# Optimization experiments

Measured on AMD Instinct MI355X. Metric: run time of the kernel, lower is better.

Reference implementation:

```python
import jax, jax.numpy as jnp
import numpy as np

L, B, N, D, H, INTER = 4, 64, 128, 1024, 16, 4096
HD = D // H
EPS = 1e-12


def layer_norm(x, g, b):
    m = jnp.mean(x, axis=-1, keepdims=True)
    v = jnp.mean(jnp.square(x - m), axis=-1, keepdims=True)
    return (x - m) * jax.lax.rsqrt(v + EPS) * g + b


def fast_self_attention(x, wq_w, wq_b, wk_w, wk_b, hwq, hwk, tr_w, tr_b):
    # x: [B, T, D]
    Bq, T, _ = x.shape
    q = x @ wq_w + wq_b                                  # [B,T,D]
    hq = q.reshape(Bq, T, H, HD).transpose(0, 2, 1, 3)    # [B,H,T,hd]
    # additive attention over queries (mask scores are all-zero here)
    alpha = jax.nn.softmax(jnp.einsum('bhtd,hd->bht', hq, hwq) / np.sqrt(HD), axis=-1)
    gq = jnp.einsum('bht,bhtd->bhd', alpha, hq).reshape(Bq, 1, D)  # global query [B,1,D]
    k = x @ wk_w + wk_b
    p = k * gq                                            # [B,T,D]
    hp = p.reshape(Bq, T, H, HD).transpose(0, 2, 1, 3)
    beta = jax.nn.softmax(jnp.einsum('bhtd,hd->bht', hp, hwk) / np.sqrt(HD), axis=-1)
    gk = jnp.einsum('bht,bhtd->bhd', beta, hp).reshape(Bq, 1, D)   # global key [B,1,D]
    u = q * gk
    r = u @ tr_w + tr_b
    return r + q


def encoder_layer(x, p, i):
    a = fast_self_attention(x, p['wq_w'][i], p['wq_b'][i], p['wk_w'][i], p['wk_b'][i],
                            p['hwq'][i], p['hwk'][i], p['tr_w'][i], p['tr_b'][i])
    a = a @ p['so_w'][i] + p['so_b'][i]
    a = layer_norm(a, p['ln1_g'][i], p['ln1_b'][i])
    h = jax.nn.gelu(a @ p['int_w'][i] + p['int_b'][i], approximate=False)
    o = h @ p['out_w'][i] + p['out_b'][i]
    return layer_norm(o + a, p['ln2_g'][i], p['ln2_b'][i])


def setup_inputs() -> dict:
    key = jax.random.key(0)
    ks = iter(jax.random.split(key, 32))
    s = 0.02
    inp = {
        'x': jax.random.normal(next(ks), (B, N, D), jnp.float32),
        'wq_w': jax.random.normal(next(ks), (L, D, D)) * s,
        'wq_b': jnp.zeros((L, D)),
        'wk_w': jax.random.normal(next(ks), (L, D, D)) * s,
        'wk_b': jnp.zeros((L, D)),
        'hwq': jax.random.normal(next(ks), (L, H, HD)) * s,
        'hwk': jax.random.normal(next(ks), (L, H, HD)) * s,
        'tr_w': jax.random.normal(next(ks), (L, D, D)) * s,
        'tr_b': jnp.zeros((L, D)),
        'so_w': jax.random.normal(next(ks), (L, D, D)) * s,
        'so_b': jnp.zeros((L, D)),
        'ln1_g': jnp.ones((L, D)),
        'ln1_b': jnp.zeros((L, D)),
        'int_w': jax.random.normal(next(ks), (L, D, INTER)) * s,
        'int_b': jnp.zeros((L, INTER)),
        'out_w': jax.random.normal(next(ks), (L, INTER, D)) * s,
        'out_b': jnp.zeros((L, D)),
        'ln2_g': jnp.ones((L, D)),
        'ln2_b': jnp.zeros((L, D)),
        'pool_w': jax.random.normal(next(ks), (D, D)) * s,
        'pool_b': jnp.zeros((D,)),
        'pool_q': jax.random.normal(next(ks), (D,)) * s,
    }
    return inp


def reference(x, wq_w, wq_b, wk_w, wk_b, hwq, hwk, tr_w, tr_b, so_w, so_b,
              ln1_g, ln1_b, int_w, int_b, out_w, out_b, ln2_g, ln2_b,
              pool_w, pool_b, pool_q):
    p = dict(wq_w=wq_w, wq_b=wq_b, wk_w=wk_w, wk_b=wk_b, hwq=hwq, hwk=hwk,
             tr_w=tr_w, tr_b=tr_b, so_w=so_w, so_b=so_b, ln1_g=ln1_g, ln1_b=ln1_b,
             int_w=int_w, int_b=int_b, out_w=out_w, out_b=out_b, ln2_g=ln2_g, ln2_b=ln2_b)
    h = x
    for i in range(L):
        h = encoder_layer(h, p, i)
    # additive attention pooling (mask scores are zeros)
    scores = jnp.tanh(h @ pool_w + pool_b) @ pool_q       # [B,N]
    w = jax.nn.softmax(scores, axis=-1)
    return jnp.einsum('bn,bnd->bd', w, h)                 # [B,D]
```

## Files before the change

### kernel.cpp

```cpp
#include <hip/hip_runtime.h>
#include <hip/hip_bf16.h>
#include <math.h>

typedef unsigned short u16;
typedef __attribute__((ext_vector_type(4))) unsigned short u16x4;
typedef __attribute__((ext_vector_type(8))) unsigned short u16x8;
typedef __attribute__((ext_vector_type(8))) short s16x8;
typedef __attribute__((ext_vector_type(4))) float f32x4;

typedef const __attribute__((address_space(1))) void* gas_t;
typedef __attribute__((address_space(3))) void* las_t;

#define DI __device__ __forceinline__

static constexpr int Bc = 64, Nc = 128, Dc = 1024, Hc = 16, HDc = 64, Ic = 4096, Lc = 4;
static constexpr int Mrows = Bc * Nc;

DI float b2f(u16 u) { union { unsigned i; float f; } x; x.i = ((unsigned)u) << 16; return x.f; }
DI u16 f2b(float f) {
  union { float f; unsigned i; } x; x.f = f;
  unsigned r = x.i + 0x7FFF + ((x.i >> 16) & 1);
  return (u16)(r >> 16);
}

#define BARRIER do { asm volatile("" ::: "memory"); __builtin_amdgcn_s_barrier(); asm volatile("" ::: "memory"); } while (0)
#define VMC(N) asm volatile("s_waitcnt vmcnt(" #N ")" ::: "memory")

#define STG(PTR, ROW0, T, SLOT) do { \
    const u16* _s = (PTR) + (size_t)((ROW0) + srow) * K + (((T) << 6) + scol); \
    __builtin_amdgcn_global_load_lds((gas_t)_s, (las_t)(smem + (SLOT) + ldsw), 16, 0, 0); \
    __builtin_amdgcn_global_load_lds((gas_t)(_s + ((size_t)K << 3)), (las_t)(smem + (SLOT) + ldsw + 1024), 16, 0, 0); \
  } while (0)

#define LDA(BUFB, RH) do { \
    _Pragma("unroll") \
    for (int mi = 0; mi < 4; ++mi) { \
      af[mi][0] = *(const s16x8*)(smem + (BUFB) + Abase_rd + (RH) * 8192 + mi * 2048 + aoff0); \
      af[mi][1] = *(const s16x8*)(smem + (BUFB) + Abase_rd + (RH) * 8192 + mi * 2048 + aoff1); \
    } } while (0)

#define LDB(DST, BUFB, CH) do { \
    _Pragma("unroll") \
    for (int nj = 0; nj < 2; ++nj) { \
      DST[nj][0] = *(const s16x8*)(smem + (BUFB) + Bbase_rd + (CH) * 4096 + nj * 2048 + aoff0); \
      DST[nj][1] = *(const s16x8*)(smem + (BUFB) + Bbase_rd + (CH) * 4096 + nj * 2048 + aoff1); \
    } } while (0)

#define MFMAQ(RH, CH, BF) do { \
    __builtin_amdgcn_s_setprio(1); \
    _Pragma("unroll") \
    for (int mi = 0; mi < 4; ++mi) \
      _Pragma("unroll") \
      for (int nj = 0; nj < 2; ++nj) { \
        acc[(RH) * 4 + mi][(CH) * 2 + nj] = __builtin_amdgcn_mfma_f32_16x16x32_bf16( \
            af[mi][0], BF[nj][0], acc[(RH) * 4 + mi][(CH) * 2 + nj], 0, 0, 0); \
        acc[(RH) * 4 + mi][(CH) * 2 + nj] = __builtin_amdgcn_mfma_f32_16x16x32_bf16( \
            af[mi][1], BF[nj][1], acc[(RH) * 4 + mi][(CH) * 2 + nj], 0, 0, 0); \
      } \
    __builtin_amdgcn_s_setprio(0); \
  } while (0)

template <int EPI, bool SPLIT>
__global__ __launch_bounds__(512, 2) void gemm256(
    const u16* __restrict__ A, const u16* __restrict__ BT,
    const float* __restrict__ bias, const float* __restrict__ bias2,
    const u16* __restrict__ resid, u16* __restrict__ C, u16* __restrict__ C2,
    int M, int N, int K, int NC) {
  extern __shared__ __align__(16) char smem[];
  const int tid = threadIdx.x;
  const int l = tid & 63;
  const int w = tid >> 6;
  const int wr = w >> 2, wc = w & 3;

  const int GX = gridDim.x;
  int wg = blockIdx.y * GX + blockIdx.x;
  const int nwg = GX * gridDim.y;
  wg = (wg & 7) * (nwg >> 3) + (wg >> 3);
  const int bn0 = (wg % GX) * 256;
  const int bm0 = (wg / GX) * 256;

  const int NT = K >> 6;
  const int NI = NT >> 1;

  const int row_l = l & 15;
  const int kl = (l >> 4) * 8;
  const int xr = (row_l & 7) << 3;
  const int aoff0 = row_l * 128 + (((0 * 32 + kl) ^ xr) * 2);
  const int aoff1 = row_l * 128 + (((1 * 32 + kl) ^ xr) * 2);
  const int Abase_rd = wr * 16384;
  const int Bbase_rd = 32768 + (wc >> 1) * 16384 + (wc & 1) * 8192;

  const int srow = w * 16 + (l >> 3);
  const int scol = ((l & 7) ^ ((l >> 3) & 7)) << 3;
  const int ldsw = w * 2048;

  enum { b0A0 = 0, b0A1 = 16384, b0B0 = 32768, b0B1 = 49152,
         b1A0 = 65536, b1A1 = 81920, b1B0 = 98304, b1B1 = 114688 };

  STG(BT, bn0, 0, b0B0);
  STG(BT, bn0 + 128, 0, b0B1);
  STG(A, bm0, 0, b0A0);
  STG(A, bm0 + 128, 0, b0A1);
  STG(BT, bn0, 1, b1B0);
  STG(BT, bn0 + 128, 1, b1B1);
  VMC(4);
  BARRIER;

  f32x4 acc[8][4];
#pragma unroll
  for (int i = 0; i < 8; ++i)
#pragma unroll
    for (int j = 0; j < 4; ++j) acc[i][j] = f32x4{0.f, 0.f, 0.f, 0.f};
  s16x8 af[4][2], bf0[2][2], bf1[2][2];

  for (int j = 0; j < NI; ++j) {
    const int t1 = 2 * j + 1;
    int t2 = 2 * j + 2; if (t2 >= NT) t2 = 0;
    int t3 = 2 * j + 3; if (t3 >= NT) t3 = 1;
    LDA(0, 0); LDB(bf0, 0, 0);
    STG(A, bm0, t1, b1A0);
    BARRIER; MFMAQ(0, 0, bf0); BARRIER;
    LDB(bf1, 0, 1);
    STG(A, bm0 + 128, t1, b1A1);
    BARRIER; MFMAQ(0, 1, bf1); BARRIER;
    LDA(0, 1);
    STG(BT, bn0, t2, b0B0);
    BARRIER; MFMAQ(1, 0, bf0); BARRIER;
    STG(BT, bn0 + 128, t2, b0B1);
    STG(A, bm0, t2, b0A0);
    VMC(6);
    BARRIER; MFMAQ(1, 1, bf1); BARRIER;
    LDA(65536, 0); LDB(bf0, 65536, 0);
    STG(A, bm0 + 128, t2, b0A1);
    BARRIER; MFMAQ(0, 0, bf0); BARRIER;
    LDB(bf1, 65536, 1);
    BARRIER; MFMAQ(0, 1, bf1); BARRIER;
    LDA(65536, 1);
    STG(BT, bn0, t3, b1B0);
    BARRIER; MFMAQ(1, 0, bf0); BARRIER;
    STG(BT, bn0 + 128, t3, b1B1);
    VMC(4);
    BARRIER; MFMAQ(1, 1, bf1); BARRIER;
  }

  u16* Cout = C;
  const float* bi = bias;
  int cb = bn0;
  if (SPLIT) {
    const int half = N >> 1;
    if (bn0 >= half) { Cout = C2; bi = bias2; cb = bn0 - half; }
  }
  const int r0 = bm0 + wr * 128 + ((l >> 4) << 2);
#pragma unroll
  for (int fi = 0; fi < 8; ++fi) {
#pragma unroll
    for (int fj = 0; fj < 4; ++fj) {
      const int ocol = cb + wc * 64 + fj * 16 + (l & 15);
      const float bv = bi[ocol];
      const int row = r0 + fi * 16;
#pragma unroll
      for (int r = 0; r < 4; ++r) {
        float v = acc[fi][fj][r] + bv;
        if constexpr (EPI == 1) v += b2f(resid[(size_t)(row + r) * NC + ocol]);
        if constexpr (EPI == 2) v = 0.5f * v * (1.f + erff(v * 0.70710678118654752f));
        if constexpr (EPI == 3) v = tanhf(v);
        Cout[(size_t)(row + r) * NC + ocol] = f2b(v);
      }
    }
  }
}

#define LDA2(BUFB, RH) do { \
    _Pragma("unroll") \
    for (int mi = 0; mi < 2; ++mi) { \
      af[mi][0] = *(const s16x8*)(smem + (BUFB) + Abase_rd + ((RH) * 2 + mi) * 2048 + aoff0); \
      af[mi][1] = *(const s16x8*)(smem + (BUFB) + Abase_rd + ((RH) * 2 + mi) * 2048 + aoff1); \
    } } while (0)

#define MFMAQ2(RH, CH, BF) do { \
    __builtin_amdgcn_s_setprio(1); \
    _Pragma("unroll") \
    for (int mi = 0; mi < 2; ++mi) \
      _Pragma("unroll") \
      for (int nj = 0; nj < 2; ++nj) { \
        acc[(RH) * 2 + mi][(CH) * 2 + nj] = __builtin_amdgcn_mfma_f32_16x16x32_bf16( \
            af[mi][0], BF[nj][0], acc[(RH) * 2 + mi][(CH) * 2 + nj], 0, 0, 0); \
        acc[(RH) * 2 + mi][(CH) * 2 + nj] = __builtin_amdgcn_mfma_f32_16x16x32_bf16( \
            af[mi][1], BF[nj][1], acc[(RH) * 2 + mi][(CH) * 2 + nj], 0, 0, 0); \
      } \
    __builtin_amdgcn_s_setprio(0); \
  } while (0)

template <int EPI>
__global__ __launch_bounds__(512, 2) void gemm128n(
    const u16* __restrict__ A, const u16* __restrict__ BT,
    const float* __restrict__ bias, const u16* __restrict__ resid,
    u16* __restrict__ C, int M, int N, int K, int NC) {
  extern __shared__ __align__(16) char smem[];
  const int tid = threadIdx.x;
  const int l = tid & 63;
  const int w = tid >> 6;
  const int wr = w >> 1, wc = w & 1;

  const int GX = gridDim.x;
  int wg = blockIdx.y * GX + blockIdx.x;
  const int nwg = GX * gridDim.y;
  wg = (wg & 7) * (nwg >> 3) + (wg >> 3);
  const int bn0 = (wg % GX) * 128;
  const int bm0 = (wg / GX) * 256;

  const int NT = K >> 6;
  const int NI = NT >> 1;

  const int row_l = l & 15;
  const int kl = (l >> 4) * 8;
  const int xr = (row_l & 7) << 3;
  const int aoff0 = row_l * 128 + (((0 * 32 + kl) ^ xr) * 2);
  const int aoff1 = row_l * 128 + (((1 * 32 + kl) ^ xr) * 2);
  const int Abase_rd = (wr >> 1) * 16384 + (wr & 1) * 8192;
  const int Bbase_rd = 32768 + wc * 8192;

  const int srow = w * 16 + (l >> 3);
  const int scol = ((l & 7) ^ ((l >> 3) & 7)) << 3;
  const int ldsw = w * 2048;

  enum { c0A0 = 0, c0A1 = 16384, c0B = 32768,
         c1A0 = 49152, c1A1 = 65536, c1B = 81920 };

  STG(BT, bn0, 0, c0B);
  STG(A, bm0, 0, c0A0);
  STG(A, bm0 + 128, 0, c0A1);
  STG(BT, bn0, 1, c1B);
  VMC(2);
  BARRIER;

  f32x4 acc[4][4];
#pragma unroll
  for (int i = 0; i < 4; ++i)
#pragma unroll
    for (int j = 0; j < 4; ++j) acc[i][j] = f32x4{0.f, 0.f, 0.f, 0.f};
  s16x8 af[2][2], bf0[2][2], bf1[2][2];

  for (int j = 0; j < NI; ++j) {
    const int t1 = 2 * j + 1;
    int t2 = 2 * j + 2; if (t2 >= NT) t2 = 0;
    int t3 = 2 * j + 3; if (t3 >= NT) t3 = 1;
    LDA2(0, 0); LDB(bf0, 0, 0);
    STG(A, bm0, t1, c1A0);
    BARRIER; MFMAQ2(0, 0, bf0); BARRIER;
    LDB(bf1, 0, 1);
    STG(A, bm0 + 128, t1, c1A1);
    BARRIER; MFMAQ2(0, 1, bf1); BARRIER;
    LDA2(0, 1);
    STG(BT, bn0, t2, c0B);
    BARRIER; MFMAQ2(1, 0, bf0); BARRIER;
    STG(A, bm0, t2, c0A0);
    VMC(4);
    BARRIER; MFMAQ2(1, 1, bf1); BARRIER;
    LDA2(49152, 0); LDB(bf0, 49152, 0);
    STG(A, bm0 + 128, t2, c0A1);
    BARRIER; MFMAQ2(0, 0, bf0); BARRIER;
    LDB(bf1, 49152, 1);
    BARRIER; MFMAQ2(0, 1, bf1); BARRIER;
    LDA2(49152, 1);
    STG(BT, bn0, t3, c1B);
    BARRIER; MFMAQ2(1, 0, bf0); BARRIER;
    VMC(2);
    BARRIER; MFMAQ2(1, 1, bf1); BARRIER;
  }

  const int r0 = bm0 + wr * 64 + ((l >> 4) << 2);
#pragma unroll
  for (int fi = 0; fi < 4; ++fi) {
#pragma unroll
    for (int fj = 0; fj < 4; ++fj) {
      const int ocol = bn0 + wc * 64 + fj * 16 + (l & 15);
      const float bv = bias[ocol];
      const int row = r0 + fi * 16;
#pragma unroll
      for (int r = 0; r < 4; ++r) {
        float v = acc[fi][fj][r] + bv;
        if constexpr (EPI == 1) v += b2f(resid[(size_t)(row + r) * NC + ocol]);
        if constexpr (EPI == 2) v = 0.5f * v * (1.f + erff(v * 0.70710678118654752f));
        if constexpr (EPI == 3) v = tanhf(v);
        C[(size_t)(row + r) * NC + ocol] = f2b(v);
      }
    }
  }
}

__global__ __launch_bounds__(256) void transpose_cvt(
    const float* __restrict__ in, u16* __restrict__ out, int R, int C) {
  __shared__ u16 tile[32][33];
  const int r0 = blockIdx.y * 32, c0 = blockIdx.x * 32;
  const int t = threadIdx.x;
  const int lr = t >> 3;
  const int lc = (t & 7) * 4;
  f32x4 v = *(const f32x4*)(in + (size_t)(r0 + lr) * C + c0 + lc);
#pragma unroll
  for (int j = 0; j < 4; ++j) tile[lr][lc + j] = f2b(v[j]);
  __syncthreads();
  u16x4 o;
#pragma unroll
  for (int j = 0; j < 4; ++j) o[j] = tile[lc + j][lr];
  *(u16x4*)(out + (size_t)(c0 + lr) * R + r0 + lc) = o;
}

__global__ __launch_bounds__(256) void cvt_k(
    const float* __restrict__ in, u16* __restrict__ out) {
  const size_t i = ((size_t)blockIdx.x * 256 + threadIdx.x) * 8;
  f32x4 a = *(const f32x4*)(in + i);
  f32x4 b = *(const f32x4*)(in + i + 4);
  u16x8 o;
#pragma unroll
  for (int j = 0; j < 4; ++j) o[j] = f2b(a[j]);
#pragma unroll
  for (int j = 0; j < 4; ++j) o[4 + j] = f2b(b[j]);
  *(u16x8*)(out + i) = o;
}

__global__ __launch_bounds__(128) void attn_gq(
    const u16* __restrict__ q, const float* __restrict__ hwq, float* __restrict__ gq) {
  const int bh = blockIdx.x;
  const int b = bh >> 4, h = bh & 15;
  const int tid = threadIdx.x;
  const int lane = tid & 63, wv = tid >> 6;
  __shared__ float hw[64];
  __shared__ float ex[128];
  __shared__ float part[64];
  __shared__ float xw[4];
  if (tid < 64) hw[tid] = hwq[h * 64 + tid];
  __syncthreads();
  const u16* row = q + ((size_t)(b * 128 + tid)) * Dc + h * 64;
  float s = 0.f;
#pragma unroll
  for (int c = 0; c < 8; ++c) {
    u16x8 v = *(const u16x8*)(row + c * 8);
#pragma unroll
    for (int j = 0; j < 8; ++j) s += b2f(v[j]) * hw[c * 8 + j];
  }
  s *= 0.125f;
  float m = s;
  for (int o = 32; o; o >>= 1) m = fmaxf(m, __shfl_xor(m, o));
  if (lane == 0) xw[wv] = m;
  __syncthreads();
  m = fmaxf(xw[0], xw[1]);
  const float e = __expf(s - m);
  ex[tid] = e;
  float sm = e;
  for (int o = 32; o; o >>= 1) sm += __shfl_xor(sm, o);
  if (lane == 0) xw[2 + wv] = sm;
  __syncthreads();
  const float sum = xw[2] + xw[3];
  const int d = tid & 63, half = tid >> 6;
  const u16* colp = q + ((size_t)(b * 128 + half * 64)) * Dc + h * 64 + d;
  float acc = 0.f;
  for (int t = 0; t < 64; ++t) acc += ex[half * 64 + t] * b2f(colp[(size_t)t * Dc]);
  if (half == 0) part[d] = acc;
  __syncthreads();
  if (half == 1) gq[b * Dc + h * 64 + d] = (part[d] + acc) / sum;
}

__global__ __launch_bounds__(128) void attn_gk(
    const u16* __restrict__ k, const float* __restrict__ hwk,
    const float* __restrict__ gq, float* __restrict__ gk) {
  const int bh = blockIdx.x;
  const int b = bh >> 4, h = bh & 15;
  const int tid = threadIdx.x;
  const int lane = tid & 63, wv = tid >> 6;
  __shared__ float hw[64];
  __shared__ float gqv[64];
  __shared__ float ex[128];
  __shared__ float part[64];
  __shared__ float xw[4];
  if (tid < 64) {
    hw[tid] = hwk[h * 64 + tid];
    gqv[tid] = gq[b * Dc + h * 64 + tid];
  }
  __syncthreads();
  const u16* row = k + ((size_t)(b * 128 + tid)) * Dc + h * 64;
  float s = 0.f;
#pragma unroll
  for (int c = 0; c < 8; ++c) {
    u16x8 v = *(const u16x8*)(row + c * 8);
#pragma unroll
    for (int j = 0; j < 8; ++j) s += b2f(v[j]) * gqv[c * 8 + j] * hw[c * 8 + j];
  }
  s *= 0.125f;
  float m = s;
  for (int o = 32; o; o >>= 1) m = fmaxf(m, __shfl_xor(m, o));
  if (lane == 0) xw[wv] = m;
  __syncthreads();
  m = fmaxf(xw[0], xw[1]);
  const float e = __expf(s - m);
  ex[tid] = e;
  float sm = e;
  for (int o = 32; o; o >>= 1) sm += __shfl_xor(sm, o);
  if (lane == 0) xw[2 + wv] = sm;
  __syncthreads();
  const float sum = xw[2] + xw[3];
  const int d = tid & 63, half = tid >> 6;
  const u16* colp = k + ((size_t)(b * 128 + half * 64)) * Dc + h * 64 + d;
  float acc = 0.f;
  for (int t = 0; t < 64; ++t) acc += ex[half * 64 + t] * b2f(colp[(size_t)t * Dc]);
  acc *= gqv[d];
  if (half == 0) part[d] = acc;
  __syncthreads();
  if (half == 1) gk[b * Dc + h * 64 + d] = (part[d] + acc) / sum;
}

__global__ __launch_bounds__(256) void mul_gk(
    const u16* __restrict__ q, const float* __restrict__ gk, u16* __restrict__ u) {
  const size_t i = ((size_t)blockIdx.x * 256 + threadIdx.x) * 8;
  const int col = (int)(i & (Dc - 1));
  const int b = (int)(i >> 17);
  u16x8 v = *(const u16x8*)(q + i);
  const float* g = gk + b * Dc + col;
  u16x8 o;
#pragma unroll
  for (int j = 0; j < 8; ++j) o[j] = f2b(b2f(v[j]) * g[j]);
  *(u16x8*)(u + i) = o;
}

__global__ __launch_bounds__(256) void ln_k(
    const u16* __restrict__ in, const float* __restrict__ g,
    const float* __restrict__ bta, u16* __restrict__ out) {
  const int row = blockIdx.x, tid = threadIdx.x;
  const int lane = tid & 63, wave = tid >> 6;
  __shared__ float red[8];
  const u16* p = in + (size_t)row * Dc + tid * 4;
  u16x4 v = *(const u16x4*)p;
  float x[4];
  float s = 0.f, sq = 0.f;
#pragma unroll
  for (int j = 0; j < 4; ++j) {
    x[j] = b2f(v[j]);
    s += x[j];
    sq += x[j] * x[j];
  }
  for (int o = 32; o; o >>= 1) {
    s += __shfl_down(s, o);
    sq += __shfl_down(sq, o);
  }
  if (lane == 0) {
    red[wave] = s;
    red[4 + wave] = sq;
  }
  __syncthreads();
  s = red[0] + red[1] + red[2] + red[3];
  sq = red[4] + red[5] + red[6] + red[7];
  const float mean = s * (1.f / 1024.f);
  const float var = sq * (1.f / 1024.f) - mean * mean;
  const float rs = rsqrtf(var + 1e-12f);
  f32x4 gv = *(const f32x4*)(g + tid * 4);
  f32x4 bv = *(const f32x4*)(bta + tid * 4);
  u16x4 o;
#pragma unroll
  for (int j = 0; j < 4; ++j) o[j] = f2b((x[j] - mean) * rs * gv[j] + bv[j]);
  *(u16x4*)(out + (size_t)row * Dc + tid * 4) = o;
}

__global__ __launch_bounds__(256) void pool_k(
    const u16* __restrict__ s1, const float* __restrict__ pq,
    const u16* __restrict__ h, float* __restrict__ out) {
  const int b = blockIdx.x, tid = threadIdx.x;
  __shared__ float pqs[1024];
  __shared__ float sc[128];
  __shared__ float ex[128];
  for (int i = tid; i < 1024; i += 256) pqs[i] = pq[i];
  __syncthreads();
  if (tid < 128) {
    const u16* row = s1 + ((size_t)(b * 128 + tid)) * Dc;
    float s = 0.f;
    for (int c = 0; c < 128; ++c) {
      u16x8 v = *(const u16x8*)(row + c * 8);
#pragma unroll
      for (int j = 0; j < 8; ++j) s += b2f(v[j]) * pqs[c * 8 + j];
    }
    sc[tid] = s;
  }
  __syncthreads();
  float m = -1e30f;
  for (int t = 0; t < 128; ++t) m = fmaxf(m, sc[t]);
  if (tid < 128) ex[tid] = __expf(sc[tid] - m);
  __syncthreads();
  float sum = 0.f;
  for (int t = 0; t < 128; ++t) sum += ex[t];
  const int d0 = tid * 4;
  float acc[4] = {0.f, 0.f, 0.f, 0.f};
  for (int n = 0; n < 128; ++n) {
    const float w = ex[n];
    u16x4 v = *(const u16x4*)(h + ((size_t)(b * 128 + n)) * Dc + d0);
#pragma unroll
    for (int j = 0; j < 4; ++j) acc[j] += w * b2f(v[j]);
  }
  const float inv = 1.f / sum;
  f32x4 o;
#pragma unroll
  for (int j = 0; j < 4; ++j) o[j] = acc[j] * inv;
  *(f32x4*)(out + b * Dc + d0) = o;
}

extern "C" void kernel_launch(void* const* d_in, const int* in_sizes, int n_in,
                              void* d_out, int out_size, void* d_ws, size_t ws_size,
                              hipStream_t stream) {
  const float* x = (const float*)d_in[0];
  const float* wq_w = (const float*)d_in[1];
  const float* wq_b = (const float*)d_in[2];
  const float* wk_w = (const float*)d_in[3];
  const float* wk_b = (const float*)d_in[4];
  const float* hwq = (const float*)d_in[5];
  const float* hwk = (const float*)d_in[6];
  const float* tr_w = (const float*)d_in[7];
  const float* tr_b = (const float*)d_in[8];
  const float* so_w = (const float*)d_in[9];
  const float* so_b = (const float*)d_in[10];
  const float* ln1g = (const float*)d_in[11];
  const float* ln1b = (const float*)d_in[12];
  const float* int_w = (const float*)d_in[13];
  const float* int_b = (const float*)d_in[14];
  const float* out_w = (const float*)d_in[15];
  const float* out_b = (const float*)d_in[16];
  const float* ln2g = (const float*)d_in[17];
  const float* ln2b = (const float*)d_in[18];
  const float* pool_w = (const float*)d_in[19];
  const float* pool_b = (const float*)d_in[20];
  const float* pool_q = (const float*)d_in[21];

  char* w = (char*)d_ws;
  auto alloc = [&](size_t bytes) {
    char* p = w;
    w += (bytes + 255) & ~(size_t)255;
    return p;
  };
  u16* wTqk = (u16*)alloc((size_t)2 * Dc * Dc * 2);
  u16* wTtr = (u16*)alloc((size_t)Dc * Dc * 2);
  u16* wTso = (u16*)alloc((size_t)Dc * Dc * 2);
  u16* wTint = (u16*)alloc((size_t)Dc * Ic * 2);
  u16* wTout = (u16*)alloc((size_t)Dc * Ic * 2);
  u16* wTpool = (u16*)alloc((size_t)Dc * Dc * 2);
  u16* qb = (u16*)alloc((size_t)Mrows * Dc * 2);
  u16* kb = (u16*)alloc((size_t)Mrows * Dc * 2);
  u16* ab = (u16*)alloc((size_t)Mrows * Dc * 2);
  u16* tb = (u16*)alloc((size_t)Mrows * Dc * 2);
  u16* xc = (u16*)alloc((size_t)Mrows * Dc * 2);
  u16* hb = (u16*)alloc((size_t)Mrows * Ic * 2);
  float* gqf = (float*)alloc((size_t)Bc * Dc * 4);
  float* gkf = (float*)alloc((size_t)Bc * Dc * 4);
  if ((size_t)(w - (char*)d_ws) > ws_size) return;

  static constexpr size_t LDSB = 131072;
  static constexpr size_t LDSB2 = 98304;
  hipFuncSetAttribute((const void*)gemm256<0, true>, hipFuncAttributeMaxDynamicSharedMemorySize, LDSB);
  hipFuncSetAttribute((const void*)gemm256<2, false>, hipFuncAttributeMaxDynamicSharedMemorySize, LDSB);
  hipFuncSetAttribute((const void*)gemm128n<0>, hipFuncAttributeMaxDynamicSharedMemorySize, LDSB2);
  hipFuncSetAttribute((const void*)gemm128n<1>, hipFuncAttributeMaxDynamicSharedMemorySize, LDSB2);
  hipFuncSetAttribute((const void*)gemm128n<3>, hipFuncAttributeMaxDynamicSharedMemorySize, LDSB2);

  const dim3 blk(256);
  const dim3 blkG(512);
  const dim3 gT1(Dc / 32, Dc / 32);
  const dim3 gTi(Ic / 32, Dc / 32);
  const dim3 gTo(Dc / 32, Ic / 32);
  const dim3 gQK(2048 / 256, Mrows / 256);
  const dim3 gNi(Ic / 256, Mrows / 256);
  const dim3 gO(Dc / 128, Mrows / 256);

  cvt_k<<<(Mrows * Dc) / (256 * 8), blk, 0, stream>>>(x, xc);

  for (int i = 0; i < Lc; ++i) {
    transpose_cvt<<<gT1, blk, 0, stream>>>(wq_w + (size_t)i * Dc * Dc, wTqk, Dc, Dc);
    transpose_cvt<<<gT1, blk, 0, stream>>>(wk_w + (size_t)i * Dc * Dc, wTqk + (size_t)Dc * Dc, Dc, Dc);
    transpose_cvt<<<gT1, blk, 0, stream>>>(tr_w + (size_t)i * Dc * Dc, wTtr, Dc, Dc);
    transpose_cvt<<<gT1, blk, 0, stream>>>(so_w + (size_t)i * Dc * Dc, wTso, Dc, Dc);
    transpose_cvt<<<gTi, blk, 0, stream>>>(int_w + (size_t)i * Dc * Ic, wTint, Dc, Ic);
    transpose_cvt<<<gTo, blk, 0, stream>>>(out_w + (size_t)i * Ic * Dc, wTout, Ic, Dc);

    gemm256<0, true><<<gQK, blkG, LDSB, stream>>>(xc, wTqk, wq_b + i * Dc, wk_b + i * Dc,
                                                  nullptr, qb, kb, Mrows, 2048, Dc, Dc);
    attn_gq<<<Bc * Hc, 128, 0, stream>>>(qb, hwq + i * Hc * HDc, gqf);
    attn_gk<<<Bc * Hc, 128, 0, stream>>>(kb, hwk + i * Hc * HDc, gqf, gkf);
    mul_gk<<<(Mrows * Dc) / (256 * 8), blk, 0, stream>>>(qb, gkf, kb);
    gemm128n<1><<<gO, blkG, LDSB2, stream>>>(kb, wTtr, tr_b + i * Dc, qb, tb, Mrows, Dc, Dc, Dc);
    gemm128n<0><<<gO, blkG, LDSB2, stream>>>(tb, wTso, so_b + i * Dc, nullptr, kb, Mrows, Dc, Dc, Dc);
    ln_k<<<Mrows, blk, 0, stream>>>(kb, ln1g + i * Dc, ln1b + i * Dc, ab);
    gemm256<2, false><<<gNi, blkG, LDSB, stream>>>(ab, wTint, int_b + i * Ic, nullptr,
                                                   nullptr, hb, nullptr, Mrows, Ic, Dc, Ic);
    gemm128n<1><<<gO, blkG, LDSB2, stream>>>(hb, wTout, out_b + i * Dc, ab, tb, Mrows, Dc, Ic, Dc);
    ln_k<<<Mrows, blk, 0, stream>>>(tb, ln2g + i * Dc, ln2b + i * Dc, xc);
  }

  transpose_cvt<<<gT1, blk, 0, stream>>>(pool_w, wTpool, Dc, Dc);
  gemm128n<3><<<gO, blkG, LDSB2, stream>>>(xc, wTpool, pool_b, nullptr, tb, Mrows, Dc, Dc, Dc);
  pool_k<<<Bc, blk, 0, stream>>>(tb, pool_q, xc, (float*)d_out);
}
```

Before: 1.274 ms.

## Stage GEMM epilogues through LDS for vectorized stores; batch weight transposes

Both GEMM kernels now write the bias-added, activated bf16 tile into swizzled LDS and then read it back as 16-byte vectors, so global stores and residual loads are coalesced rows instead of scattered 2-byte accesses. The residual add now happens after the bf16 rounding of the GEMM result, which adds a second rounding step. The six per-layer weight transpose launches are also merged into two launches using blockIdx.z. This cuts launch overhead and uncoalesced epilogue traffic, at the cost of extra barriers and an LDS round trip.

```diff
diff --git a/kernel.cpp b/kernel.cpp
--- a/kernel.cpp
+++ b/kernel.cpp
@@ -25,6 +25,7 @@
 
 #define BARRIER do { asm volatile("" ::: "memory"); __builtin_amdgcn_s_barrier(); asm volatile("" ::: "memory"); } while (0)
 #define VMC(N) asm volatile("s_waitcnt vmcnt(" #N ")" ::: "memory")
+#define LGKM0 asm volatile("s_waitcnt lgkmcnt(0)" ::: "memory")
 
 #define STG(PTR, ROW0, T, SLOT) do { \
     const u16* _s = (PTR) + (size_t)((ROW0) + srow) * K + (((T) << 6) + scol); \
@@ -143,6 +144,10 @@
     BARRIER; MFMAQ(1, 1, bf1); BARRIER;
   }
 
+  VMC(0);
+  LGKM0;
+  BARRIER;
+
   u16* Cout = C;
   const float* bi = bias;
   int cb = bn0;
@@ -150,22 +155,44 @@
     const int half = N >> 1;
     if (bn0 >= half) { Cout = C2; bi = bias2; cb = bn0 - half; }
   }
-  const int r0 = bm0 + wr * 128 + ((l >> 4) << 2);
+  const int lcol = l & 15;
+  const int lrow4 = (l >> 4) << 2;
 #pragma unroll
   for (int fi = 0; fi < 8; ++fi) {
 #pragma unroll
     for (int fj = 0; fj < 4; ++fj) {
-      const int ocol = cb + wc * 64 + fj * 16 + (l & 15);
-      const float bv = bi[ocol];
-      const int row = r0 + fi * 16;
+      const int col = wc * 64 + fj * 16 + lcol;
+      const float bv = bi[cb + col];
 #pragma unroll
       for (int r = 0; r < 4; ++r) {
+        const int row = wr * 128 + fi * 16 + lrow4 + r;
         float v = acc[fi][fj][r] + bv;
-        if constexpr (EPI == 1) v += b2f(resid[(size_t)(row + r) * NC + ocol]);
         if constexpr (EPI == 2) v = 0.5f * v * (1.f + erff(v * 0.70710678118654752f));
         if constexpr (EPI == 3) v = tanhf(v);
-        Cout[(size_t)(row + r) * NC + ocol] = f2b(v);
+        int byt = (row << 9) + (col << 1);
+        byt ^= (row & 12) << 3;
+        *(u16*)(smem + byt) = f2b(v);
       }
+    }
+  }
+  LGKM0;
+  BARRIER;
+#pragma unroll
+  for (int it = 0; it < 16; ++it) {
+    const int rr = w * 32 + it * 2 + (l >> 5);
+    int byt = (rr << 9) + ((l & 31) << 4);
+    byt ^= (rr & 12) << 3;
+    u16x8 vv = *(const u16x8*)(smem + byt);
+    u16* dst = Cout + (size_t)(bm0 + rr) * NC + cb + ((l & 31) << 3);
+    if constexpr (EPI == 1) {
+      const u16* rs = resid + (size_t)(bm0 + rr) * NC + cb + ((l & 31) << 3);
+      u16x8 rv = *(const u16x8*)rs;
+      u16x8 ov;
+#pragma unroll
+      for (int q = 0; q < 8; ++q) ov[q] = f2b(b2f(vv[q]) + b2f(rv[q]));
+      *(u16x8*)dst = ov;
+    } else {
+      *(u16x8*)dst = vv;
     }
   }
 }
@@ -269,31 +296,53 @@
     BARRIER; MFMAQ2(1, 1, bf1); BARRIER;
   }
 
-  const int r0 = bm0 + wr * 64 + ((l >> 4) << 2);
+  VMC(0);
+  LGKM0;
+  BARRIER;
+  const int lcol = l & 15;
+  const int lrow4 = (l >> 4) << 2;
 #pragma unroll
   for (int fi = 0; fi < 4; ++fi) {
 #pragma unroll
     for (int fj = 0; fj < 4; ++fj) {
-      const int ocol = bn0 + wc * 64 + fj * 16 + (l & 15);
-      const float bv = bias[ocol];
-      const int row = r0 + fi * 16;
+      const int col = wc * 64 + fj * 16 + lcol;
+      const float bv = bias[bn0 + col];
 #pragma unroll
       for (int r = 0; r < 4; ++r) {
+        const int row = wr * 64 + fi * 16 + lrow4 + r;
         float v = acc[fi][fj][r] + bv;
-        if constexpr (EPI == 1) v += b2f(resid[(size_t)(row + r) * NC + ocol]);
         if constexpr (EPI == 2) v = 0.5f * v * (1.f + erff(v * 0.70710678118654752f));
         if constexpr (EPI == 3) v = tanhf(v);
-        C[(size_t)(row + r) * NC + ocol] = f2b(v);
+        int byt = (row << 8) + (col << 1);
+        byt ^= (row & 12) << 3;
+        *(u16*)(smem + byt) = f2b(v);
       }
     }
   }
-}
-
-__global__ __launch_bounds__(256) void transpose_cvt(
-    const float* __restrict__ in, u16* __restrict__ out, int R, int C) {
+  LGKM0;
+  BARRIER;
+#pragma unroll
+  for (int it = 0; it < 8; ++it) {
+    const int rr = w * 32 + it * 4 + (l >> 4);
+    int byt = (rr << 8) + ((l & 15) << 4);
+    byt ^= (rr & 12) << 3;
+    u16x8 vv = *(const u16x8*)(smem + byt);
+    u16* dst = C + (size_t)(bm0 + rr) * NC + bn0 + ((l & 15) << 3);
+    if constexpr (EPI == 1) {
+      const u16* rs = resid + (size_t)(bm0 + rr) * NC + bn0 + ((l & 15) << 3);
+      u16x8 rv = *(const u16x8*)rs;
+      u16x8 ov;
+#pragma unroll
+      for (int q = 0; q < 8; ++q) ov[q] = f2b(b2f(vv[q]) + b2f(rv[q]));
+      *(u16x8*)dst = ov;
+    } else {
+      *(u16x8*)dst = vv;
+    }
+  }
+}
+
+DI void ttile(const float* in, u16* out, int R, int C, int r0, int c0, int t) {
   __shared__ u16 tile[32][33];
-  const int r0 = blockIdx.y * 32, c0 = blockIdx.x * 32;
-  const int t = threadIdx.x;
   const int lr = t >> 3;
   const int lc = (t & 7) * 4;
   f32x4 v = *(const f32x4*)(in + (size_t)(r0 + lr) * C + c0 + lc);
@@ -304,6 +353,29 @@
 #pragma unroll
   for (int j = 0; j < 4; ++j) o[j] = tile[lc + j][lr];
   *(u16x4*)(out + (size_t)(c0 + lr) * R + r0 + lc) = o;
+}
+
+__global__ __launch_bounds__(256) void transpose_cvt(
+    const float* __restrict__ in, u16* __restrict__ out, int R, int C) {
+  ttile(in, out, R, C, blockIdx.y * 32, blockIdx.x * 32, threadIdx.x);
+}
+
+__global__ __launch_bounds__(256) void transpose4sq(
+    const float* s0, const float* s1, const float* s2, const float* s3,
+    u16* d0, u16* d1, u16* d2, u16* d3) {
+  const int z = blockIdx.z;
+  const float* in = z == 0 ? s0 : z == 1 ? s1 : z == 2 ? s2 : s3;
+  u16* out = z == 0 ? d0 : z == 1 ? d1 : z == 2 ? d2 : d3;
+  ttile(in, out, 1024, 1024, blockIdx.y * 32, blockIdx.x * 32, threadIdx.x);
+}
+
+__global__ __launch_bounds__(256) void transpose_io(
+    const float* si, u16* di, const float* so, u16* dout) {
+  if (blockIdx.z == 0) {
+    ttile(si, di, 1024, 4096, blockIdx.y * 32, blockIdx.x * 32, threadIdx.x);
+  } else {
+    ttile(so, dout, 4096, 1024, blockIdx.x * 32, blockIdx.y * 32, threadIdx.x);
+  }
 }
 
 __global__ __launch_bounds__(256) void cvt_k(
@@ -560,8 +632,8 @@
   const dim3 blk(256);
   const dim3 blkG(512);
   const dim3 gT1(Dc / 32, Dc / 32);
-  const dim3 gTi(Ic / 32, Dc / 32);
-  const dim3 gTo(Dc / 32, Ic / 32);
+  const dim3 gT4(Dc / 32, Dc / 32, 4);
+  const dim3 gTio(Ic / 32, Dc / 32, 2);
   const dim3 gQK(2048 / 256, Mrows / 256);
   const dim3 gNi(Ic / 256, Mrows / 256);
   const dim3 gO(Dc / 128, Mrows / 256);
@@ -569,12 +641,12 @@
   cvt_k<<<(Mrows * Dc) / (256 * 8), blk, 0, stream>>>(x, xc);
 
   for (int i = 0; i < Lc; ++i) {
-    transpose_cvt<<<gT1, blk, 0, stream>>>(wq_w + (size_t)i * Dc * Dc, wTqk, Dc, Dc);
-    transpose_cvt<<<gT1, blk, 0, stream>>>(wk_w + (size_t)i * Dc * Dc, wTqk + (size_t)Dc * Dc, Dc, Dc);
-    transpose_cvt<<<gT1, blk, 0, stream>>>(tr_w + (size_t)i * Dc * Dc, wTtr, Dc, Dc);
-    transpose_cvt<<<gT1, blk, 0, stream>>>(so_w + (size_t)i * Dc * Dc, wTso, Dc, Dc);
-    transpose_cvt<<<gTi, blk, 0, stream>>>(int_w + (size_t)i * Dc * Ic, wTint, Dc, Ic);
-    transpose_cvt<<<gTo, blk, 0, stream>>>(out_w + (size_t)i * Ic * Dc, wTout, Ic, Dc);
+    transpose4sq<<<gT4, blk, 0, stream>>>(
+        wq_w + (size_t)i * Dc * Dc, wk_w + (size_t)i * Dc * Dc,
+        tr_w + (size_t)i * Dc * Dc, so_w + (size_t)i * Dc * Dc,
+        wTqk, wTqk + (size_t)Dc * Dc, wTtr, wTso);
+    transpose_io<<<gTio, blk, 0, stream>>>(
+        int_w + (size_t)i * Dc * Ic, wTint, out_w + (size_t)i * Ic * Dc, wTout);
 
     gemm256<0, true><<<gQK, blkG, LDSB, stream>>>(xc, wTqk, wq_b + i * Dc, wk_b + i * Dc,
                                                   nullptr, qb, kb, Mrows, 2048, Dc, Dc);
```

New measurement: 1.294 ms. No clear change (+1.6%).
